# Kernel optimization log

Measured on AMD Instinct MI355X. Metric: run time of the kernel, lower is better.

Reference implementation:

```python
import jax, jax.numpy as jnp
import numpy as np

BETA = 0.25


def setup_inputs() -> dict:
    key = jax.random.key(0)
    k1, k2, k3, k4 = jax.random.split(key, 4)
    e_dim, n_e = 512, 8192
    z = jax.random.normal(k1, (16, e_dim, 32, 32), dtype=jnp.float32)
    # nn.init.normal_(embedding.weight, std=e_dim**-0.5)
    emb_weight = jax.random.normal(k2, (n_e, e_dim), dtype=jnp.float32) * (e_dim ** -0.5)
    # torch Linear default init ~ U(-1/sqrt(in), 1/sqrt(in))
    lim = 1.0 / np.sqrt(e_dim)
    proj_w = jax.random.uniform(k3, (e_dim, e_dim), minval=-lim, maxval=lim, dtype=jnp.float32)
    proj_b = jax.random.uniform(k4, (e_dim,), minval=-lim, maxval=lim, dtype=jnp.float32)
    return {"z": z, "emb_weight": emb_weight, "proj_w": proj_w, "proj_b": proj_b}


def reference(z, emb_weight, proj_w, proj_b):
    # z: [B, C, H, W] -> [B, H, W, C]
    zc = jnp.transpose(z, (0, 2, 3, 1))
    B, H, W, C = zc.shape
    z_flat = zc.reshape(-1, C)                               # [N, C]
    # projected codebook: Linear(e_dim, e_dim) -> x @ W^T + b
    qc = emb_weight @ proj_w.T + proj_b                      # [n_e, C]
    # squared distances: ||z||^2 + ||qc||^2 - 2 z.qc
    d = (jnp.sum(z_flat ** 2, axis=1, keepdims=True)
         + jnp.sum(qc ** 2, axis=1)
         - 2.0 * jnp.einsum('nd,kd->nk', z_flat, qc))        # [N, n_e]
    idx = jnp.argmin(d, axis=1)                              # [N]
    z_q = qc[idx].reshape(zc.shape)                          # [B, H, W, C]
    # legacy=False commit loss
    commit_loss = (BETA * jnp.mean((jax.lax.stop_gradient(z_q) - zc) ** 2)
                   + jnp.mean((z_q - jax.lax.stop_gradient(zc)) ** 2))
    # straight-through
    z_q = zc + jax.lax.stop_gradient(z_q - zc)
    z_q = jnp.transpose(z_q, (0, 3, 1, 2))                   # [B, C, H, W]
    min_encoding_indices = idx.reshape(B, H, W)              # sane_index_shape=True
    return z_q, commit_loss, min_encoding_indices
```

## Files before the change

### kernel.cpp

```cpp
#include <hip/hip_runtime.h>

typedef unsigned int uint;
typedef unsigned short ushort;
typedef unsigned long long ulong64;
typedef __attribute__((ext_vector_type(8))) short short8;
typedef __attribute__((ext_vector_type(4))) float f32x4;

#define B_   16
#define C_   512
#define HW_  1024
#define N_   16384
#define K_   8192
#define EPS_ 0.25f

#define QC_OFF    0u
#define QC_SZ     (K_ * C_)
#define QN_OFF    (QC_OFF + QC_SZ)
#define QN_SZ     K_
#define ZN_OFF    (QN_OFF + QN_SZ)
#define ZN_SZ     N_
#define ZF_OFF    (ZN_OFF + ZN_SZ)
#define ZF_SZ     (N_ * C_)
#define ZH_OFF    (ZF_OFF + ZF_SZ)
#define ZH_SZ     (N_ * C_ / 2)
#define QH_OFF    (ZH_OFF + ZH_SZ)
#define QH_SZ     (K_ * C_ / 2)
#define WT_OFF    (QH_OFF + QH_SZ)
#define WT_SZ     (64 * N_ * 4)
#define IDXF_OFF  (WT_OFF + WT_SZ)
#define IDXF_SZ   N_
#define LOSS_OFF  (IDXF_OFF + IDXF_SZ)

#define OUT_ZQ    0
#define OUT_LOSS  8388608
#define OUT_IDX   8388609

__device__ __forceinline__ ushort f2bf(float f) {
    uint x = __float_as_uint(f);
    uint r = x + 0x7fffu + ((x >> 16) & 1u);
    return (ushort)(r >> 16);
}

__global__ __launch_bounds__(256) void fused_front(const float* __restrict__ z,
                                                   const float* __restrict__ emb,
                                                   const float* __restrict__ W,
                                                   const float* __restrict__ bias,
                                                   float* __restrict__ qc,
                                                   ushort* __restrict__ qh,
                                                   float* __restrict__ zf,
                                                   ushort* __restrict__ zh,
                                                   float* __restrict__ zn) {
    __shared__ float smem[4160];
    const int blk = blockIdx.x;
    const int t   = threadIdx.x;

    if (blk < 512) {
        float (*As)[132] = (float(*)[132])smem;
        float (*Bs)[68]  = (float(*)[68])(smem + 16 * 132);
        const int k0   = (blk >> 3) * 128;
        const int c0   = (blk & 7) * 64;
        const int ty   = t >> 4, tx = t & 15;
        const int rowA = t >> 1;
        const int dqA  = (t & 1) * 8;
        const int rowB = t >> 2;
        const int dqB  = (t & 3) * 4;

        const float* pa = emb + (size_t)(k0 + rowA) * 512 + dqA;
        const float* pb = W   + (size_t)(c0 + rowB) * 512 + dqB;
        float4 ra0 = *(const float4*)&pa[0];
        float4 ra1 = *(const float4*)&pa[4];
        float4 rb  = *(const float4*)&pb[0];

        float acc[2][4][4] = {};
        for (int d0 = 0; d0 < 512; d0 += 16) {
            __syncthreads();
            As[dqA + 0][rowA] = ra0.x; As[dqA + 1][rowA] = ra0.y;
            As[dqA + 2][rowA] = ra0.z; As[dqA + 3][rowA] = ra0.w;
            As[dqA + 4][rowA] = ra1.x; As[dqA + 5][rowA] = ra1.y;
            As[dqA + 6][rowA] = ra1.z; As[dqA + 7][rowA] = ra1.w;
            Bs[dqB + 0][rowB] = rb.x;  Bs[dqB + 1][rowB] = rb.y;
            Bs[dqB + 2][rowB] = rb.z;  Bs[dqB + 3][rowB] = rb.w;
            if (d0 + 16 < 512) {
                ra0 = *(const float4*)&pa[d0 + 16];
                ra1 = *(const float4*)&pa[d0 + 20];
                rb  = *(const float4*)&pb[d0 + 16];
            }
            __syncthreads();
#pragma unroll
            for (int dd = 0; dd < 16; ++dd) {
                float4 a0 = *(const float4*)&As[dd][ty * 4];
                float4 a1 = *(const float4*)&As[dd][64 + ty * 4];
                float4 b0 = *(const float4*)&Bs[dd][tx * 4];
                float aa[2][4] = {{a0.x, a0.y, a0.z, a0.w}, {a1.x, a1.y, a1.z, a1.w}};
                float bb[4] = {b0.x, b0.y, b0.z, b0.w};
#pragma unroll
                for (int ih = 0; ih < 2; ++ih)
#pragma unroll
                    for (int i = 0; i < 4; ++i)
#pragma unroll
                        for (int j = 0; j < 4; ++j)
                            acc[ih][i][j] += aa[ih][i] * bb[j];
            }
        }
#pragma unroll
        for (int ih = 0; ih < 2; ++ih)
#pragma unroll
            for (int i = 0; i < 4; ++i) {
                const size_t kr = (size_t)(k0 + ih * 64 + ty * 4 + i) * 512;
                const int cb = c0 + tx * 4;
                float4 v;
                v.x = acc[ih][i][0] + bias[cb + 0];
                v.y = acc[ih][i][1] + bias[cb + 1];
                v.z = acc[ih][i][2] + bias[cb + 2];
                v.w = acc[ih][i][3] + bias[cb + 3];
                *(float4*)&qc[kr + cb] = v;
                ushort4 h; h.x = f2bf(v.x); h.y = f2bf(v.y); h.z = f2bf(v.z); h.w = f2bf(v.w);
                *(ushort4*)&qh[kr + cb] = h;
            }
    } else if (blk < 2560) {
        float (*ld)[65] = (float(*)[65])smem;
        const int i  = blk - 512;
        const int mt = i & 15, ct = (i >> 4) & 7, b = i >> 7;
        {
            const int cl = t >> 4, m4 = (t & 15) * 4;
#pragma unroll
            for (int cc = 0; cc < 4; ++cc) {
                const int c = ct * 64 + cc * 16 + cl;
                float4 v = *(const float4*)&z[((size_t)(b * 512 + c)) * 1024 + mt * 64 + m4];
                ld[cc * 16 + cl][m4 + 0] = v.x; ld[cc * 16 + cl][m4 + 1] = v.y;
                ld[cc * 16 + cl][m4 + 2] = v.z; ld[cc * 16 + cl][m4 + 3] = v.w;
            }
        }
        __syncthreads();
        {
            const int nl = t >> 4, c4 = (t & 15) * 4;
#pragma unroll
            for (int nn = 0; nn < 4; ++nn) {
                const int n_local = nn * 16 + nl;
                const size_t n = (size_t)b * 1024 + mt * 64 + n_local;
                float4 w;
                w.x = ld[c4 + 0][n_local]; w.y = ld[c4 + 1][n_local];
                w.z = ld[c4 + 2][n_local]; w.w = ld[c4 + 3][n_local];
                *(float4*)&zf[n * 512 + ct * 64 + c4] = w;
                ushort4 h; h.x = f2bf(w.x); h.y = f2bf(w.y); h.z = f2bf(w.z); h.w = f2bf(w.w);
                *(ushort4*)&zh[n * 512 + ct * 64 + c4] = h;
            }
        }
    } else {
#pragma clang fp contract(off)
        const int n = (blk - 2560) * 256 + t;
        const int b = n >> 10, m = n & 1023;
        const float* base = z + (size_t)b * C_ * HW_ + m;
        float s128[4];
#pragma unroll
        for (int bk = 0; bk < 4; ++bk) {
            float r[8];
#pragma unroll
            for (int j = 0; j < 8; ++j) {
                float v = base[(size_t)(bk * 128 + j) * HW_];
                r[j] = v * v;
            }
#pragma unroll 1
            for (int i = 8; i < 128; i += 8) {
#pragma unroll
                for (int j = 0; j < 8; ++j) {
                    float v = base[(size_t)(bk * 128 + i + j) * HW_];
                    float sq = v * v;
                    r[j] = r[j] + sq;
                }
            }
            s128[bk] = ((r[0] + r[1]) + (r[2] + r[3])) + ((r[4] + r[5]) + (r[6] + r[7]));
        }
        zn[n] = (s128[0] + s128[1]) + (s128[2] + s128[3]);
    }
}

__global__ __launch_bounds__(256) void qnorm_grouped(const float* __restrict__ qc,
                                                     float* __restrict__ qn) {
#pragma clang fp contract(off)
    const int t   = threadIdx.x;
    const int grp = t >> 3;
    const int j   = t & 7;
    const int k   = blockIdx.x * 32 + grp;
    const float* row = qc + (size_t)k * C_;
    float s[4];
#pragma unroll
    for (int blk = 0; blk < 4; ++blk) {
        float v0 = row[blk * 128 + j];
        float r  = v0 * v0;
#pragma unroll 1
        for (int i = 1; i < 16; ++i) {
            float v  = row[blk * 128 + i * 8 + j];
            float sq = v * v;
            r = r + sq;
        }
        float t1 = r  + __shfl_xor(r, 1, 64);
        float t2 = t1 + __shfl_xor(t1, 2, 64);
        float t3 = t2 + __shfl_xor(t2, 4, 64);
        s[blk] = t3;
    }
    if (j == 0) qn[k] = (s[0] + s[1]) + (s[2] + s[3]);
}

#define PH_BAR()   __builtin_amdgcn_s_barrier()
#define PH_LGKM()  asm volatile("s_waitcnt lgkmcnt(0)" ::: "memory")
#define PH_VM4()   asm volatile("s_waitcnt vmcnt(4)" ::: "memory")
#define PH_VM0()   asm volatile("s_waitcnt vmcnt(0)" ::: "memory")

__device__ __forceinline__ short8 ld8(const short* p, int off) {
    return *(const short8*)(p + off);
}

__global__ __launch_bounds__(512, 2) void phaseA(const ushort* __restrict__ qh,
                                                 const ushort* __restrict__ zh,
                                                 const float* __restrict__ qn,
                                                 float* __restrict__ wtop) {
    __shared__ short lq[32768];
    __shared__ short lz[32768];
    const int t    = threadIdx.x;
    const int lane = t & 63;
    const int wv   = t >> 6;
    const int wk   = wv >> 2;
    const int wn   = wv & 3;
    const int n0   = blockIdx.x * 256;

    const int l15 = lane & 15;
    const int hi8 = (lane >> 4) << 3;
    const int xr  = (l15 & 7) << 3;
    const short* pA0 = lq + wk * 8192 + l15 * 64 + ((hi8) ^ xr);
    const short* pA1 = lq + wk * 8192 + l15 * 64 + ((32 + hi8) ^ xr);
    const short* pB0 = lz + (wn >> 1) * 8192 + (wn & 1) * 4096 + l15 * 64 + ((hi8) ^ xr);
    const short* pB1 = lz + (wn >> 1) * 8192 + (wn & 1) * 4096 + l15 * 64 + ((32 + hi8) ^ xr);

    const int ch0 = t,        row0 = ch0 >> 3;
    const int ch1 = t + 512,  row1 = ch1 >> 3;
    const int ce0 = ((ch0 ^ row0) & 7) << 3;
    const int ce1 = ((ch1 ^ row1) & 7) << 3;
    const ushort* qsrc0 = qh + (size_t)row0 * 512 + ce0;
    const ushort* qsrc1 = qh + (size_t)row1 * 512 + ce1;
    const ushort* zsrc0 = zh + (size_t)(n0 + row0) * 512 + ce0;
    const ushort* zsrc1 = zh + (size_t)(n0 + row1) * 512 + ce1;
    short* qdst0 = lq + ch0 * 8;
    short* qdst1 = lq + ch1 * 8;
    short* zdst0 = lz + ch0 * 8;
    short* zdst1 = lz + ch1 * 8;

    size_t koff = (size_t)blockIdx.y * 8 * 131072;

    auto stage_half = [&](int b, int h, int ci) {
        if (h < 2) {
            const size_t co = koff + (size_t)((ci & 7) * 64 + (ci >> 3) * 131072);
            __builtin_amdgcn_global_load_lds(
                (const __attribute__((address_space(1))) uint*)(qsrc0 + h * 65536 + co),
                (__attribute__((address_space(3))) uint*)(qdst0 + (b * 2 + h) * 8192), 16, 0, 0);
            __builtin_amdgcn_global_load_lds(
                (const __attribute__((address_space(1))) uint*)(qsrc1 + h * 65536 + co),
                (__attribute__((address_space(3))) uint*)(qdst1 + (b * 2 + h) * 8192), 16, 0, 0);
        } else {
            const int co = (ci & 7) * 64;
            __builtin_amdgcn_global_load_lds(
                (const __attribute__((address_space(1))) uint*)(zsrc0 + (h - 2) * 65536 + co),
                (__attribute__((address_space(3))) uint*)(zdst0 + (b * 2 + (h - 2)) * 8192), 16, 0, 0);
            __builtin_amdgcn_global_load_lds(
                (const __attribute__((address_space(1))) uint*)(zsrc1 + (h - 2) * 65536 + co),
                (__attribute__((address_space(3))) uint*)(zdst1 + (b * 2 + (h - 2)) * 8192), 16, 0, 0);
        }
    };

    f32x4 acc[8][4];
    short8 a0[2][4], a1[2][4], b0[2][2], b1[2][2];

    stage_half(0, 0, 0); stage_half(0, 1, 0); stage_half(0, 2, 0); stage_half(0, 3, 0);
    stage_half(1, 0, 1); stage_half(1, 1, 1);
    PH_VM4();
    PH_BAR();

#pragma unroll 1
    for (int yp = 0; yp < 8; ++yp) {
        koff = (size_t)(blockIdx.y * 8 + yp) * 131072;
        const int k0e = (blockIdx.y * 8 + yp) * 256;

#pragma unroll
        for (int i = 0; i < 8; ++i)
#pragma unroll
            for (int j = 0; j < 4; ++j) acc[i][j] = (f32x4){0.f, 0.f, 0.f, 0.f};

#pragma unroll 1
        for (int I = 0; I < 4; ++I) {
            const int t1 = 2 * I + 1;
            const int t2 = 2 * I + 2;
            const int t3 = 2 * I + 3;

#pragma unroll
            for (int i = 0; i < 4; ++i) {
                a0[0][i] = ld8(pA0, i * 1024);        a0[1][i] = ld8(pA1, i * 1024);
                a1[0][i] = ld8(pA0, 4096 + i * 1024); a1[1][i] = ld8(pA1, 4096 + i * 1024);
            }
#pragma unroll
            for (int jj = 0; jj < 2; ++jj) { b0[0][jj] = ld8(pB0, jj * 1024); b0[1][jj] = ld8(pB1, jj * 1024); }
            stage_half(1, 2, t1); stage_half(1, 3, t1);
            PH_BAR();
            __builtin_amdgcn_s_setprio(1);
#pragma unroll
            for (int kk = 0; kk < 2; ++kk)
#pragma unroll
                for (int i = 0; i < 4; ++i)
#pragma unroll
                    for (int jj = 0; jj < 2; ++jj) {
                        acc[i][jj]     = __builtin_amdgcn_mfma_f32_16x16x32_bf16(a0[kk][i], b0[kk][jj], acc[i][jj], 0, 0, 0);
                        acc[4 + i][jj] = __builtin_amdgcn_mfma_f32_16x16x32_bf16(a1[kk][i], b0[kk][jj], acc[4 + i][jj], 0, 0, 0);
                    }
            __builtin_amdgcn_s_setprio(0);
            PH_LGKM();
            PH_BAR();
#pragma unroll
            for (int jj = 0; jj < 2; ++jj) { b1[0][jj] = ld8(pB0, 2048 + jj * 1024); b1[1][jj] = ld8(pB1, 2048 + jj * 1024); }
            stage_half(0, 0, t2); stage_half(0, 1, t2);
            PH_BAR();
            __builtin_amdgcn_s_setprio(1);
#pragma unroll
            for (int kk = 0; kk < 2; ++kk)
#pragma unroll
                for (int i = 0; i < 4; ++i)
#pragma unroll
                    for (int jj = 0; jj < 2; ++jj) {
                        acc[i][2 + jj]     = __builtin_amdgcn_mfma_f32_16x16x32_bf16(a0[kk][i], b1[kk][jj], acc[i][2 + jj], 0, 0, 0);
                        acc[4 + i][2 + jj] = __builtin_amdgcn_mfma_f32_16x16x32_bf16(a1[kk][i], b1[kk][jj], acc[4 + i][2 + jj], 0, 0, 0);
                    }
            __builtin_amdgcn_s_setprio(0);
            PH_LGKM();
            PH_VM4();
            PH_BAR();

#pragma unroll
            for (int i = 0; i < 4; ++i) {
                a0[0][i] = ld8(pA0, 16384 + i * 1024);        a0[1][i] = ld8(pA1, 16384 + i * 1024);
                a1[0][i] = ld8(pA0, 16384 + 4096 + i * 1024); a1[1][i] = ld8(pA1, 16384 + 4096 + i * 1024);
            }
#pragma unroll
            for (int jj = 0; jj < 2; ++jj) { b0[0][jj] = ld8(pB0, 16384 + jj * 1024); b0[1][jj] = ld8(pB1, 16384 + jj * 1024); }
            stage_half(0, 2, t2); stage_half(0, 3, t2);
            PH_BAR();
            __builtin_amdgcn_s_setprio(1);
#pragma unroll
            for (int kk = 0; kk < 2; ++kk)
#pragma unroll
                for (int i = 0; i < 4; ++i)
#pragma unroll
                    for (int jj = 0; jj < 2; ++jj) {
                        acc[i][jj]     = __builtin_amdgcn_mfma_f32_16x16x32_bf16(a0[kk][i], b0[kk][jj], acc[i][jj], 0, 0, 0);
                        acc[4 + i][jj] = __builtin_amdgcn_mfma_f32_16x16x32_bf16(a1[kk][i], b0[kk][jj], acc[4 + i][jj], 0, 0, 0);
                    }
            __builtin_amdgcn_s_setprio(0);
            PH_LGKM();
            PH_BAR();
#pragma unroll
            for (int jj = 0; jj < 2; ++jj) { b1[0][jj] = ld8(pB0, 16384 + 2048 + jj * 1024); b1[1][jj] = ld8(pB1, 16384 + 2048 + jj * 1024); }
            stage_half(1, 0, t3); stage_half(1, 1, t3);
            PH_BAR();
            __builtin_amdgcn_s_setprio(1);
#pragma unroll
            for (int kk = 0; kk < 2; ++kk)
#pragma unroll
                for (int i = 0; i < 4; ++i)
#pragma unroll
                    for (int jj = 0; jj < 2; ++jj) {
                        acc[i][2 + jj]     = __builtin_amdgcn_mfma_f32_16x16x32_bf16(a0[kk][i], b1[kk][jj], acc[i][2 + jj], 0, 0, 0);
                        acc[4 + i][2 + jj] = __builtin_amdgcn_mfma_f32_16x16x32_bf16(a1[kk][i], b1[kk][jj], acc[4 + i][2 + jj], 0, 0, 0);
                    }
            __builtin_amdgcn_s_setprio(0);
            PH_LGKM();
            if (I == 3) { PH_VM0(); } else { PH_VM4(); }
            PH_BAR();
        }

        const int q4 = (lane >> 4) * 4;
        float v1[4], v2[4];
        int   k1[4], k2[4];
#pragma unroll
        for (int in = 0; in < 4; ++in) { v1[in] = 1e30f; v2[in] = 1e30f; k1[in] = 0; k2[in] = 0; }

#pragma unroll
        for (int ik = 0; ik < 8; ++ik) {
            float qv[4];
#pragma unroll
            for (int r = 0; r < 4; ++r)
                qv[r] = qn[k0e + wk * 128 + ik * 16 + q4 + r];
#pragma unroll
            for (int in = 0; in < 4; ++in) {
#pragma unroll
                for (int r = 0; r < 4; ++r) {
                    const float val = qv[r] - 2.0f * acc[ik][in][r];
                    const int   kg  = k0e + wk * 128 + ik * 16 + q4 + r;
                    if (val < v1[in]) { v2[in] = v1[in]; k2[in] = k1[in]; v1[in] = val; k1[in] = kg; }
                    else if (val < v2[in]) { v2[in] = val; k2[in] = kg; }
                }
            }
        }
#pragma unroll
        for (int m = 16; m <= 32; m <<= 1) {
#pragma unroll
            for (int in = 0; in < 4; ++in) {
                const float ov1 = __shfl_xor(v1[in], m, 64);
                const int   ok1 = __shfl_xor(k1[in], m, 64);
                const float ov2 = __shfl_xor(v2[in], m, 64);
                const int   ok2 = __shfl_xor(k2[in], m, 64);
                float nv1, nv2; int nk1, nk2;
                if (ov1 < v1[in]) {
                    nv1 = ov1; nk1 = ok1;
                    if (v1[in] < ov2) { nv2 = v1[in]; nk2 = k1[in]; } else { nv2 = ov2; nk2 = ok2; }
                } else {
                    nv1 = v1[in]; nk1 = k1[in];
                    if (ov1 < v2[in]) { nv2 = ov1; nk2 = ok1; } else { nv2 = v2[in]; nk2 = k2[in]; }
                }
                v1[in] = nv1; k1[in] = nk1; v2[in] = nv2; k2[in] = nk2;
            }
        }
        if ((lane >> 4) == 0) {
            const int w = (blockIdx.y * 8 + yp) * 2 + wk;
#pragma unroll
            for (int in = 0; in < 4; ++in) {
                const int n = n0 + wn * 64 + in * 16 + (lane & 15);
                float4 o; o.x = v1[in]; o.y = __int_as_float(k1[in]);
                o.z = v2[in]; o.w = __int_as_float(k2[in]);
                *(float4*)&wtop[((size_t)n * 64 + w) * 4] = o;
            }
        }
    }
}

__global__ __launch_bounds__(256) void phaseBC(const float* __restrict__ zf,
                                               const float* __restrict__ qc,
                                               const float* __restrict__ zn,
                                               const float* __restrict__ qn,
                                               const float* __restrict__ wtop,
                                               int* __restrict__ idxf,
                                               float* __restrict__ out_idx,
                                               float* __restrict__ loss_acc) {
    __shared__ float zr[4][512];
    __shared__ float ql[4][2][512];
    __shared__ int   clist[4][128];
    const int wv   = threadIdx.x >> 6;
    const int lane = threadIdx.x & 63;
    const int r    = blockIdx.x * 4 + wv;
    if (blockIdx.x == 0 && threadIdx.x == 0) loss_acc[0] = 0.f;

    float4 e = *(const float4*)&wtop[((size_t)r * 64 + lane) * 4];
    float rmin = e.x;
#pragma unroll
    for (int m = 1; m <= 32; m <<= 1) rmin = fminf(rmin, __shfl_xor(rmin, m, 64));
    const float thr = rmin + EPS_;
    const bool h1 = (e.x <= thr), h2 = (e.z <= thr);
    const ulong64 m1 = __ballot(h1);
    const ulong64 m2 = __ballot(h2);
    const int c1  = __popcll(m1);
    const int cnt = c1 + __popcll(m2);

    if (cnt == 1) {
        if (h1) { const int k = __float_as_int(e.y); idxf[r] = k; out_idx[r] = (float)k; }
        else if (h2) { const int k = __float_as_int(e.w); idxf[r] = k; out_idx[r] = (float)k; }
        return;
    }

    const ulong64 below = (lane == 63) ? ~0ull >> 1 : ((1ull << lane) - 1);
    if (h1) clist[wv][__popcll(m1 & below)] = __float_as_int(e.y);
    if (h2) clist[wv][c1 + __popcll(m2 & below)] = __float_as_int(e.w);

    *(float4*)&zr[wv][lane * 8]     = *(const float4*)&zf[(size_t)r * 512 + lane * 8];
    *(float4*)&zr[wv][lane * 8 + 4] = *(const float4*)&zf[(size_t)r * 512 + lane * 8 + 4];
    asm volatile("s_waitcnt lgkmcnt(0)" ::: "memory");

    const int g  = lane >> 5;
    const int cl = (lane & 31) * 16;
    const int steps = (cnt + 1) >> 1;
    const float znr = zn[r];

    auto cand_of = [&](int s) {
        const int ci = 2 * s + g;
        return clist[wv][ci < cnt ? ci : 0];
    };

    int k_cur = cand_of(0);
    const float* q0 = qc + (size_t)k_cur * 512 + cl;
    float4 p0 = *(const float4*)&q0[0];
    float4 p1 = *(const float4*)&q0[4];
    float4 p2 = *(const float4*)&q0[8];
    float4 p3 = *(const float4*)&q0[12];

    float bd = 1e30f;
    int   bi = 0x7fffffff;

    for (int s = 0; s < steps; ++s) {
        *(float4*)&ql[wv][g][cl + 0]  = p0;
        *(float4*)&ql[wv][g][cl + 4]  = p1;
        *(float4*)&ql[wv][g][cl + 8]  = p2;
        *(float4*)&ql[wv][g][cl + 12] = p3;

        int k_next = 0;
        if (s + 1 < steps) {
            k_next = cand_of(s + 1);
            const float* qn_ = qc + (size_t)k_next * 512 + cl;
            p0 = *(const float4*)&qn_[0];
            p1 = *(const float4*)&qn_[4];
            p2 = *(const float4*)&qn_[8];
            p3 = *(const float4*)&qn_[12];
        }

        float acc = 0.f;
#pragma unroll 16
        for (int c = 0; c < 512; c += 4) {
            float4 zv = *(const float4*)&zr[wv][c];
            float4 qv = *(const float4*)&ql[wv][g][c];
            acc = fmaf(zv.x, qv.x, acc);
            acc = fmaf(zv.y, qv.y, acc);
            acc = fmaf(zv.z, qv.z, acc);
            acc = fmaf(zv.w, qv.w, acc);
        }
        const float T = znr + qn[k_cur];
        const float d = T - 2.0f * acc;
        const bool valid = (2 * s + g) < cnt;
        if (valid && (d < bd || (d == bd && k_cur < bi))) { bd = d; bi = k_cur; }
        k_cur = k_next;
    }

    const float od = __shfl_xor(bd, 32, 64);
    const int   oi = __shfl_xor(bi, 32, 64);
    if (od < bd || (od == bd && oi < bi)) { bd = od; bi = oi; }

    if (lane == 0) { idxf[r] = bi; out_idx[r] = (float)bi; }
}

__global__ __launch_bounds__(256) void gather_out(const float* __restrict__ z,
                                                  const float* __restrict__ qc,
                                                  const int* __restrict__ idxf,
                                                  float* __restrict__ zq_out,
                                                  float* __restrict__ loss_acc) {
    __shared__ int   idxs[64];
    __shared__ float zqs[64][65];
    __shared__ float wsum[4];
    const int t  = threadIdx.x;
    const int mc = blockIdx.x;
    const int cc = blockIdx.y;
    const int bz = blockIdx.z;

    if (t < 64) idxs[t] = idxf[bz * 1024 + mc * 64 + t];
    __syncthreads();
    {
        const int row  = t >> 2;
        const int coff = (t & 3) * 16;
        const float* src = qc + (size_t)idxs[row] * 512 + cc * 64 + coff;
#pragma unroll
        for (int v = 0; v < 4; ++v) {
            float4 q = *(const float4*)&src[v * 4];
            zqs[row][coff + v * 4 + 0] = q.x;
            zqs[row][coff + v * 4 + 1] = q.y;
            zqs[row][coff + v * 4 + 2] = q.z;
            zqs[row][coff + v * 4 + 3] = q.w;
        }
    }
    __syncthreads();

    float ls = 0.f;
    {
        const int c_local = t >> 2;
        const int mg      = (t & 3) * 16;
        const size_t gbase = ((size_t)(bz * 512 + cc * 64 + c_local)) * 1024 + mc * 64 + mg;
#pragma unroll
        for (int v = 0; v < 4; ++v) {
            const int m = mg + v * 4;
            float4 w;
            w.x = zqs[m + 0][c_local];
            w.y = zqs[m + 1][c_local];
            w.z = zqs[m + 2][c_local];
            w.w = zqs[m + 3][c_local];
            float4 zv = *(const float4*)&z[gbase + v * 4];
            float dx = w.x - zv.x, dy = w.y - zv.y, dz = w.z - zv.z, dw = w.w - zv.w;
            ls += dx * dx + dy * dy + dz * dz + dw * dw;
            *(float4*)&zq_out[gbase + v * 4] = w;
        }
    }
#pragma unroll
    for (int m = 32; m; m >>= 1) ls += __shfl_xor(ls, m, 64);
    const int lane = t & 63, wvv = t >> 6;
    if (lane == 0) wsum[wvv] = ls;
    __syncthreads();
    if (t == 0) atomicAdd(loss_acc, wsum[0] + wsum[1] + wsum[2] + wsum[3]);
}

__global__ void finalize(const float* __restrict__ loss_acc,
                         float* __restrict__ out_loss) {
    out_loss[0] = 1.25f * loss_acc[0] / 8388608.0f;
}

extern "C" void kernel_launch(void* const* d_in, const int* in_sizes, int n_in,
                              void* d_out, int out_size, void* d_ws, size_t ws_size,
                              hipStream_t stream) {
    const float* z    = (const float*)d_in[0];
    const float* emb  = (const float*)d_in[1];
    const float* W    = (const float*)d_in[2];
    const float* bias = (const float*)d_in[3];
    float* ws = (float*)d_ws;

    float*  qc       = ws + QC_OFF;
    float*  qn       = ws + QN_OFF;
    float*  zn       = ws + ZN_OFF;
    float*  zf       = ws + ZF_OFF;
    ushort* zh       = (ushort*)(ws + ZH_OFF);
    ushort* qh       = (ushort*)(ws + QH_OFF);
    float*  wtop     = ws + WT_OFF;
    int*    idxf     = (int*)(ws + IDXF_OFF);
    float*  loss_acc = ws + LOSS_OFF;
    float*  out      = (float*)d_out;

    fused_front<<<2624, 256, 0, stream>>>(z, emb, W, bias, qc, qh, zf, zh, zn);
    qnorm_grouped<<<K_ / 32, 256, 0, stream>>>(qc, qn);
    phaseA<<<dim3(N_ / 256, 4), 512, 0, stream>>>(qh, zh, qn, wtop);
    phaseBC<<<N_ / 4, 256, 0, stream>>>(zf, qc, zn, qn, wtop, idxf, out + OUT_IDX, loss_acc);
    gather_out<<<dim3(16, 8, B_), 256, 0, stream>>>(z, qc, idxf, out + OUT_ZQ, loss_acc);
    finalize<<<1, 1, 0, stream>>>(loss_acc, out + OUT_LOSS);
}
```

Before: 366.4 us.

## Simplify phaseA GEMM pipeline to whole-tile double buffering with one barrier per step

Replaces the fine-grained half-tile staging schedule (several barriers per k-step, vmcnt(4) partial waits) with a plain double-buffered loop. Each iteration issues all four stage loads for the next tile, reads the full A/B fragments for the current buffer, runs all MFMAs, then waits vmcnt(0) and barriers once. Fewer barriers cut sync overhead, but the loads now get less time to overlap with compute because each iteration fully drains before the next starts. Fragment register pressure also rises since b0 and b1 are loaded together.

```diff
diff --git a/kernel.cpp b/kernel.cpp
--- a/kernel.cpp
+++ b/kernel.cpp
@@ -204,7 +204,6 @@
 
 #define PH_BAR()   __builtin_amdgcn_s_barrier()
 #define PH_LGKM()  asm volatile("s_waitcnt lgkmcnt(0)" ::: "memory")
-#define PH_VM4()   asm volatile("s_waitcnt vmcnt(4)" ::: "memory")
 #define PH_VM0()   asm volatile("s_waitcnt vmcnt(0)" ::: "memory")
 
 __device__ __forceinline__ short8 ld8(const short* p, int off) {
@@ -271,8 +270,7 @@
     short8 a0[2][4], a1[2][4], b0[2][2], b1[2][2];
 
     stage_half(0, 0, 0); stage_half(0, 1, 0); stage_half(0, 2, 0); stage_half(0, 3, 0);
-    stage_half(1, 0, 1); stage_half(1, 1, 1);
-    PH_VM4();
+    PH_VM0();
     PH_BAR();
 
 #pragma unroll 1
@@ -286,20 +284,25 @@
             for (int j = 0; j < 4; ++j) acc[i][j] = (f32x4){0.f, 0.f, 0.f, 0.f};
 
 #pragma unroll 1
-        for (int I = 0; I < 4; ++I) {
-            const int t1 = 2 * I + 1;
-            const int t2 = 2 * I + 2;
-            const int t3 = 2 * I + 3;
+        for (int I = 0; I < 8; ++I) {
+            const int bo = (I & 1) * 16384;
+            const int nb = (I + 1) & 1;
+            const int ci = I + 1;
+
+            stage_half(nb, 0, ci); stage_half(nb, 1, ci);
+            stage_half(nb, 2, ci); stage_half(nb, 3, ci);
 
 #pragma unroll
             for (int i = 0; i < 4; ++i) {
-                a0[0][i] = ld8(pA0, i * 1024);        a0[1][i] = ld8(pA1, i * 1024);
-                a1[0][i] = ld8(pA0, 4096 + i * 1024); a1[1][i] = ld8(pA1, 4096 + i * 1024);
-            }
-#pragma unroll
-            for (int jj = 0; jj < 2; ++jj) { b0[0][jj] = ld8(pB0, jj * 1024); b0[1][jj] = ld8(pB1, jj * 1024); }
-            stage_half(1, 2, t1); stage_half(1, 3, t1);
-            PH_BAR();
+                a0[0][i] = ld8(pA0, bo + i * 1024);        a0[1][i] = ld8(pA1, bo + i * 1024);
+                a1[0][i] = ld8(pA0, bo + 4096 + i * 1024); a1[1][i] = ld8(pA1, bo + 4096 + i * 1024);
+            }
+#pragma unroll
+            for (int jj = 0; jj < 2; ++jj) {
+                b0[0][jj] = ld8(pB0, bo + jj * 1024);        b0[1][jj] = ld8(pB1, bo + jj * 1024);
+                b1[0][jj] = ld8(pB0, bo + 2048 + jj * 1024); b1[1][jj] = ld8(pB1, bo + 2048 + jj * 1024);
+            }
+
             __builtin_amdgcn_s_setprio(1);
 #pragma unroll
             for (int kk = 0; kk < 2; ++kk)
@@ -310,14 +313,6 @@
                         acc[i][jj]     = __builtin_amdgcn_mfma_f32_16x16x32_bf16(a0[kk][i], b0[kk][jj], acc[i][jj], 0, 0, 0);
                         acc[4 + i][jj] = __builtin_amdgcn_mfma_f32_16x16x32_bf16(a1[kk][i], b0[kk][jj], acc[4 + i][jj], 0, 0, 0);
                     }
-            __builtin_amdgcn_s_setprio(0);
-            PH_LGKM();
-            PH_BAR();
-#pragma unroll
-            for (int jj = 0; jj < 2; ++jj) { b1[0][jj] = ld8(pB0, 2048 + jj * 1024); b1[1][jj] = ld8(pB1, 2048 + jj * 1024); }
-            stage_half(0, 0, t2); stage_half(0, 1, t2);
-            PH_BAR();
-            __builtin_amdgcn_s_setprio(1);
 #pragma unroll
             for (int kk = 0; kk < 2; ++kk)
 #pragma unroll
@@ -328,49 +323,9 @@
                         acc[4 + i][2 + jj] = __builtin_amdgcn_mfma_f32_16x16x32_bf16(a1[kk][i], b1[kk][jj], acc[4 + i][2 + jj], 0, 0, 0);
                     }
             __builtin_amdgcn_s_setprio(0);
+
             PH_LGKM();
-            PH_VM4();
-            PH_BAR();
-
-#pragma unroll
-            for (int i = 0; i < 4; ++i) {
-                a0[0][i] = ld8(pA0, 16384 + i * 1024);        a0[1][i] = ld8(pA1, 16384 + i * 1024);
-                a1[0][i] = ld8(pA0, 16384 + 4096 + i * 1024); a1[1][i] = ld8(pA1, 16384 + 4096 + i * 1024);
-            }
-#pragma unroll
-            for (int jj = 0; jj < 2; ++jj) { b0[0][jj] = ld8(pB0, 16384 + jj * 1024); b0[1][jj] = ld8(pB1, 16384 + jj * 1024); }
-            stage_half(0, 2, t2); stage_half(0, 3, t2);
-            PH_BAR();
-            __builtin_amdgcn_s_setprio(1);
-#pragma unroll
-            for (int kk = 0; kk < 2; ++kk)
-#pragma unroll
-                for (int i = 0; i < 4; ++i)
-#pragma unroll
-                    for (int jj = 0; jj < 2; ++jj) {
-                        acc[i][jj]     = __builtin_amdgcn_mfma_f32_16x16x32_bf16(a0[kk][i], b0[kk][jj], acc[i][jj], 0, 0, 0);
-                        acc[4 + i][jj] = __builtin_amdgcn_mfma_f32_16x16x32_bf16(a1[kk][i], b0[kk][jj], acc[4 + i][jj], 0, 0, 0);
-                    }
-            __builtin_amdgcn_s_setprio(0);
-            PH_LGKM();
-            PH_BAR();
-#pragma unroll
-            for (int jj = 0; jj < 2; ++jj) { b1[0][jj] = ld8(pB0, 16384 + 2048 + jj * 1024); b1[1][jj] = ld8(pB1, 16384 + 2048 + jj * 1024); }
-            stage_half(1, 0, t3); stage_half(1, 1, t3);
-            PH_BAR();
-            __builtin_amdgcn_s_setprio(1);
-#pragma unroll
-            for (int kk = 0; kk < 2; ++kk)
-#pragma unroll
-                for (int i = 0; i < 4; ++i)
-#pragma unroll
-                    for (int jj = 0; jj < 2; ++jj) {
-                        acc[i][2 + jj]     = __builtin_amdgcn_mfma_f32_16x16x32_bf16(a0[kk][i], b1[kk][jj], acc[i][2 + jj], 0, 0, 0);
-                        acc[4 + i][2 + jj] = __builtin_amdgcn_mfma_f32_16x16x32_bf16(a1[kk][i], b1[kk][jj], acc[4 + i][2 + jj], 0, 0, 0);
-                    }
-            __builtin_amdgcn_s_setprio(0);
-            PH_LGKM();
-            if (I == 3) { PH_VM0(); } else { PH_VM4(); }
+            PH_VM0();
             PH_BAR();
         }
 
```

New measurement: 377.6 us. +3.1%, slower.
